# Optimization experiments

Measured on AMD Instinct MI355X. Metric: run time of the kernel, lower is better.

The kernel has to match this reference:

```python
import jax, jax.numpy as jnp
import numpy as np

EMBED_DIM = 128
NUM_SYMBOLS = 200000
PAD_IDX = NUM_SYMBOLS
K_NEIGHBORS = 10
PROCESS_STEPS = 4
D_MODEL = 2 * EMBED_DIM   # 256
D_INNER = 2 * D_MODEL     # 512
LSTM_HID = 2 * D_MODEL    # 512
B, F_SUP, MAX_K = 4096, 5, 64


def setup_inputs() -> dict:
    key = jax.random.key(0)
    ks = jax.random.split(key, 40)
    f = lambda i, shape, s=0.05: jax.random.normal(ks[i], shape, jnp.float32) * s
    inp = {}
    inp['query'] = jax.random.randint(ks[0], (B, 2), 0, NUM_SYMBOLS)
    inp['support'] = jax.random.randint(ks[1], (F_SUP, 2), 0, NUM_SYMBOLS)
    inp['q_l1'] = jax.random.randint(ks[2], (B, MAX_K, 2), 0, NUM_SYMBOLS + 1)
    inp['q_deg_l'] = jax.random.randint(ks[3], (B,), 0, 100)
    inp['q_r1'] = jax.random.randint(ks[4], (B, MAX_K, 2), 0, NUM_SYMBOLS + 1)
    inp['q_deg_r'] = jax.random.randint(ks[5], (B,), 0, 100)
    inp['s_l1'] = jax.random.randint(ks[6], (F_SUP, MAX_K, 2), 0, NUM_SYMBOLS + 1)
    inp['s_deg_l'] = jax.random.randint(ks[7], (F_SUP,), 0, 100)
    inp['s_r1'] = jax.random.randint(ks[8], (F_SUP, MAX_K, 2), 0, NUM_SYMBOLS + 1)
    inp['s_deg_r'] = jax.random.randint(ks[9], (F_SUP,), 0, 100)
    # learned parameters
    inp['symbol_emb'] = f(10, (NUM_SYMBOLS + 1, EMBED_DIM), 0.1).at[PAD_IDX].set(0.0)
    inp['gcn_w_w'] = f(11, (EMBED_DIM, 2 * EMBED_DIM))
    inp['gcn_w_b'] = jnp.zeros((EMBED_DIM,), jnp.float32)
    inp['gcn_b'] = jnp.zeros((EMBED_DIM,), jnp.float32)
    inp['g1_w'] = f(12, (EMBED_DIM // 2, EMBED_DIM))
    inp['g1_b'] = jnp.zeros((EMBED_DIM // 2,), jnp.float32)
    inp['ln1_g'] = jnp.ones((EMBED_DIM // 2,), jnp.float32)
    inp['ln1_b'] = jnp.zeros((EMBED_DIM // 2,), jnp.float32)
    inp['g2_w'] = f(13, (1, EMBED_DIM // 2))
    inp['g2_b'] = jnp.zeros((1,), jnp.float32)
    inp['gate_temp'] = jnp.array(1.0, jnp.float32)
    inp['se_p1_w'] = f(14, (D_INNER, D_MODEL))
    inp['se_p1_b'] = jnp.zeros((D_INNER,), jnp.float32)
    inp['se_p2_w'] = f(15, (D_MODEL, D_INNER))
    inp['se_p2_b'] = jnp.zeros((D_MODEL,), jnp.float32)
    inp['se_ln_g'] = jnp.ones((D_MODEL,), jnp.float32)
    inp['se_ln_b'] = jnp.zeros((D_MODEL,), jnp.float32)
    inp['w_ih'] = f(16, (4 * LSTM_HID, D_MODEL))
    inp['w_hh'] = f(17, (4 * LSTM_HID, LSTM_HID))
    inp['b_ih'] = jnp.zeros((4 * LSTM_HID,), jnp.float32)
    inp['b_hh'] = jnp.zeros((4 * LSTM_HID,), jnp.float32)
    return inp


def _layernorm(x, g, b, eps=1e-5):
    m = jnp.mean(x, axis=-1, keepdims=True)
    v = jnp.var(x, axis=-1, keepdims=True)
    return (x - m) / jnp.sqrt(v + eps) * g + b


def _l2norm(x):
    return x / jnp.maximum(jnp.linalg.norm(x, axis=-1, keepdims=True), 1e-12)


def _neighbor_encoder(conn, deg, self_ids, p):
    emb = p['symbol_emb']
    rel, ent = conn[:, :, 0], conn[:, :, 1]
    rel_emb = emb[rel]            # [n, K, D] gather
    ent_emb = emb[ent]            # [n, K, D]
    self_emb = emb[self_ids]      # [n, D]
    sim = jnp.einsum('nd,nkd->nk', _l2norm(self_emb), _l2norm(ent_emb))
    is_pad = (rel == PAD_IDX).astype(jnp.float32)
    sim = sim - is_pad * 1e9
    k = min(K_NEIGHBORS, conn.shape[1])
    _, k_idx = jax.lax.top_k(sim, k)
    bidx = jnp.arange(conn.shape[0])[:, None]
    k_mask = jnp.zeros(sim.shape, jnp.float32).at[bidx, k_idx].set(1.0)[..., None]
    concat = jnp.concatenate([rel_emb, ent_emb], axis=-1)   # [n, K, 2D]
    proj = jax.nn.leaky_relu(concat @ p['gcn_w_w'].T + p['gcn_w_b'] + p['gcn_b'], 0.01)
    valid = (1.0 - is_pad[..., None]) * k_mask
    denom = jnp.maximum(jnp.sum(valid, axis=1), 1.0)
    agg = jnp.sum((proj * k_mask) * valid, axis=1) / denom   # [n, D]
    h = jax.nn.relu(_layernorm(agg @ p['g1_w'].T + p['g1_b'], p['ln1_g'], p['ln1_b']))
    logit = h @ p['g2_w'].T + p['g2_b']                      # [n, 1]
    temp = jnp.clip(p['gate_temp'], 0.1, 5.0)
    gate = jax.nn.sigmoid(logit / temp) * (deg > 0).astype(jnp.float32)[:, None]
    return jnp.tanh(self_emb + gate * agg)


def _support_encoder(x, p):
    h = jax.nn.relu(x @ p['se_p1_w'].T + p['se_p1_b'])
    h = h @ p['se_p2_w'].T + p['se_p2_b']
    return _layernorm(h + x, p['se_ln_g'], p['se_ln_b'])


def _query_encoder(support, query, p):
    n = query.shape[0]
    h_r0 = jnp.zeros((n, LSTM_HID), jnp.float32)
    c0 = jnp.zeros((n, LSTM_HID), jnp.float32)

    def step(carry, _):
        h_r, c = carry
        gates = query @ p['w_ih'].T + p['b_ih'] + h_r @ p['w_hh'].T + p['b_hh']
        i, f, g, o = jnp.split(gates, 4, axis=-1)
        c = jax.nn.sigmoid(f) * c + jax.nn.sigmoid(i) * jnp.tanh(g)
        h_ = jax.nn.sigmoid(o) * jnp.tanh(c)
        h = query + h_[:, :D_MODEL]
        attn = jax.nn.softmax(h @ support.T, axis=1)
        r = attn @ support
        return (jnp.concatenate([h, r], axis=-1), c), None

    (h_r, _), _ = jax.lax.scan(step, (h_r0, c0), None, length=PROCESS_STEPS)
    return h_r[:, :D_MODEL]


def reference(query, support, q_l1, q_deg_l, q_r1, q_deg_r, s_l1, s_deg_l, s_r1, s_deg_r,
              symbol_emb, gcn_w_w, gcn_w_b, gcn_b, g1_w, g1_b, ln1_g, ln1_b, g2_w, g2_b,
              gate_temp, se_p1_w, se_p1_b, se_p2_w, se_p2_b, se_ln_g, se_ln_b,
              w_ih, w_hh, b_ih, b_hh):
    p = dict(symbol_emb=symbol_emb, gcn_w_w=gcn_w_w, gcn_w_b=gcn_w_b, gcn_b=gcn_b,
             g1_w=g1_w, g1_b=g1_b, ln1_g=ln1_g, ln1_b=ln1_b, g2_w=g2_w, g2_b=g2_b,
             gate_temp=gate_temp, se_p1_w=se_p1_w, se_p1_b=se_p1_b, se_p2_w=se_p2_w,
             se_p2_b=se_p2_b, se_ln_g=se_ln_g, se_ln_b=se_ln_b,
             w_ih=w_ih, w_hh=w_hh, b_ih=b_ih, b_hh=b_hh)
    q_left = _neighbor_encoder(q_l1, q_deg_l, query[:, 0], p)
    q_right = _neighbor_encoder(q_r1, q_deg_r, query[:, 1], p)
    query_vec = jnp.concatenate([q_left, q_right], axis=-1)      # [B, 2D]
    s_left = _neighbor_encoder(s_l1, s_deg_l, support[:, 0], p)
    s_right = _neighbor_encoder(s_r1, s_deg_r, support[:, 1], p)
    support_vec = jnp.concatenate([s_left, s_right], axis=-1)    # [F, 2D]
    support_g = jnp.mean(_support_encoder(support_vec, p), axis=0, keepdims=True)  # [1, 2D]
    query_enc = _support_encoder(query_vec, p)                   # [B, 2D]
    query_g = _query_encoder(support_g, query_enc, p)            # [B, 2D]
    return jnp.sum(query_g * support_g, axis=1)                  # [B]
```

## Files before the change

kernel.cpp:

```cpp
#include <hip/hip_runtime.h>
#include <math.h>

#define BQ 4096
#define F_SUP 5
#define MAXK 64
#define ED 128
#define DM 256
#define DI 512
#define LH 512
#define NG 2048
#define PADX 200000
#define KNB 10
#define MROWS 82048
#define MREAL 82020
#define MQ 4224
#define EMB_ELEMS 25600128
#define NEMB8 3200016

typedef unsigned short u16;
typedef __attribute__((ext_vector_type(8))) short short8;
typedef __attribute__((ext_vector_type(4))) float floatx4;

__device__ __forceinline__ float sigf(float x) { return 1.0f / (1.0f + __expf(-x)); }
__device__ __forceinline__ float tanh_fast(float x) {
  float a = fabsf(x);
  float e = __expf(-2.0f * a);
  float t = (1.0f - e) / (1.0f + e);
  return copysignf(t, x);
}
__device__ __forceinline__ u16 f2bf(float f) {
  unsigned u = __float_as_uint(f);
  unsigned r = (u + 0x7FFFu + ((u >> 16) & 1u)) >> 16;
  return (u16)r;
}
__device__ __forceinline__ float bf2f(u16 u) {
  return __uint_as_float(((unsigned)u) << 16);
}
__device__ __forceinline__ void gl2lds16(const void* g, void* l) {
  __builtin_amdgcn_global_load_lds(
      (const __attribute__((address_space(1))) void*)g,
      (__attribute__((address_space(3))) void*)l, 16, 0, 0);
}

__global__ __launch_bounds__(256) void prep_all(
    const float* __restrict__ emb, u16* __restrict__ embb,
    const float* __restrict__ p1, const float* __restrict__ p2,
    const float* __restrict__ gcnw, const float* __restrict__ wih,
    const float* __restrict__ whh, const float* __restrict__ bih,
    const float* __restrict__ bhh,
    u16* __restrict__ p1b, u16* __restrict__ p2b, u16* __restrict__ gcnb,
    u16* __restrict__ wihb, u16* __restrict__ whhb, float* __restrict__ bihh,
    float* __restrict__ outz)
{
  long gid = (long)blockIdx.x * 256 + threadIdx.x;
  if (gid < (long)NEMB8) {
    long i = gid * 8;
    float4 f0 = *(const float4*)(emb + i);
    float4 f1 = *(const float4*)(emb + i + 4);
    short8 s;
    s[0]=(short)f2bf(f0.x); s[1]=(short)f2bf(f0.y); s[2]=(short)f2bf(f0.z); s[3]=(short)f2bf(f0.w);
    s[4]=(short)f2bf(f1.x); s[5]=(short)f2bf(f1.y); s[6]=(short)f2bf(f1.z); s[7]=(short)f2bf(f1.w);
    *(short8*)(embb + i) = s;
    return;
  }
  int g2 = (int)(gid - NEMB8);
  if (g2 < 131072) { p1b[g2] = f2bf(p1[g2]); }
  else if (g2 < 262144) { int i = g2 - 131072; p2b[i] = f2bf(p2[i]); }
  else if (g2 < 294912) { int i = g2 - 262144; gcnb[i] = f2bf(gcnw[i]); }
  else if (g2 < 819200) {
    int i = g2 - 294912; int p = i >> 8, k = i & 255;
    int g = (p >> 4) & 3, uu = (p >> 7) * 32 + ((p >> 6) & 1) * 16 + (p & 15);
    int n = g * 512 + uu;
    wihb[i] = f2bf(wih[(long)n * DM + k]);
  } else if (g2 < 1343488) {
    int i = g2 - 819200; int p = i >> 8, k = i & 255;
    int g = (p >> 4) & 3, uu = (p >> 7) * 32 + ((p >> 6) & 1) * 16 + (p & 15);
    int n = g * 512 + uu;
    whhb[i] = f2bf(whh[(long)n * LH + k]);
  } else if (g2 < 1345536) {
    int p = g2 - 1343488;
    int g = (p >> 4) & 3, uu = (p >> 7) * 32 + ((p >> 6) & 1) * 16 + (p & 15);
    int n = g * 512 + uu;
    bihh[p] = bih[n] + bhh[n];
  } else if (g2 < 1345536 + BQ) {
    outz[g2 - 1345536] = 0.f;
  }
}

__global__ __launch_bounds__(256) void nbr_simrank_kernel(
    const int* __restrict__ query, const int* __restrict__ support,
    const int* __restrict__ q_l1, const int* __restrict__ q_r1,
    const int* __restrict__ s_l1, const int* __restrict__ s_r1,
    const u16* __restrict__ embb, int* __restrict__ idxA, int* __restrict__ meta)
{
  __shared__ float sE[128];
  __shared__ float simS[64];
  __shared__ int relS[64], entS[64];
  int tid = threadIdx.x;
  int b = blockIdx.x;
  const int* conn; int self_id;
  if (b < BQ)              { int i = b;              conn = q_l1 + (long)i*(MAXK*2); self_id = query[2*i];   }
  else if (b < 2*BQ)       { int i = b - BQ;         conn = q_r1 + (long)i*(MAXK*2); self_id = query[2*i+1]; }
  else if (b < 2*BQ+F_SUP) { int i = b - 2*BQ;       conn = s_l1 + (long)i*(MAXK*2); self_id = support[2*i]; }
  else                     { int i = b - 2*BQ-F_SUP; conn = s_r1 + (long)i*(MAXK*2); self_id = support[2*i+1]; }

  int k = tid >> 2, part = tid & 3;
  int2 rc = *(const int2*)(conn + 2 * k);
  if (tid < 16) {
    short8 s = *(const short8*)(embb + (long)self_id * ED + tid * 8);
    #pragma unroll
    for (int j = 0; j < 8; ++j) sE[tid * 8 + j] = bf2f((u16)s[j]);
  }
  __syncthreads();

  const u16* er = embb + (long)rc.y * ED + part * 8;
  float dot = 0.f, sq = 0.f;
  #pragma unroll
  for (int i = 0; i < 4; ++i) {
    short8 e8 = *(const short8*)(er + i * 32);
    #pragma unroll
    for (int j = 0; j < 8; ++j) {
      float e = bf2f((u16)e8[j]);
      float s = sE[i * 32 + part * 8 + j];
      dot += e * s; sq += e * e;
    }
  }
  dot += __shfl_xor(dot, 1); dot += __shfl_xor(dot, 2);
  sq  += __shfl_xor(sq, 1);  sq  += __shfl_xor(sq, 2);
  if (part == 0) {
    float ne = fmaxf(sqrtf(sq), 1e-12f);
    float sim = dot / ne;
    if (rc.x == PADX) sim -= 1e9f;
    simS[k] = sim; relS[k] = rc.x; entS[k] = rc.y;
  }
  __syncthreads();

  if (tid < 64) {
    float my = simS[tid];
    int rank = 0;
    #pragma unroll
    for (int j = 0; j < 64; ++j) {
      float s = simS[j];
      rank += ((s > my) || (s == my && j < tid)) ? 1 : 0;
    }
    bool val = (rank < KNB) && (relS[tid] != PADX);
    unsigned long long vm = __ballot(val ? 1 : 0);
    int cnt = __popcll(vm);
    long base = (long)b * 10;
    if (val) {
      int pos = __popcll(vm & ((1ull << tid) - 1ull));
      int2 p; p.x = relS[tid]; p.y = entS[tid];
      *(int2*)(idxA + (base + pos) * 2) = p;
    }
    if (tid >= cnt && tid < KNB) {
      int2 pp; pp.x = PADX; pp.y = PADX;
      *(int2*)(idxA + (base + tid) * 2) = pp;
    }
    if (tid == 0) meta[b] = cnt;
  }
  if (b == 0 && tid >= 64 && tid < 64 + 2 * (MROWS - MREAL)) {
    idxA[(long)MREAL * 2 + (tid - 64)] = PADX;
  }
}

__global__ __launch_bounds__(256) void proj_gather_gemm(
    const int* __restrict__ idxA, const u16* __restrict__ embb,
    const u16* __restrict__ W, u16* __restrict__ proj)
{
  __shared__ u16 As[128 * 32];
  __shared__ u16 Bs[128 * 32];
  __shared__ int idxS[256];
  int tid = threadIdx.x;
  int bm = blockIdx.x;
  idxS[tid] = idxA[bm * 256 + tid];
  int lane = tid & 63, wave = tid >> 6;
  int wm = (wave & 1) * 64, wn = (wave >> 1) * 64;
  int col = lane & 15, quad = lane >> 4;

  floatx4 acc[4][4];
  #pragma unroll
  for (int i = 0; i < 4; ++i)
    #pragma unroll
    for (int j = 0; j < 4; ++j) { floatx4 z = {0.f,0.f,0.f,0.f}; acc[i][j] = z; }
  __syncthreads();

  for (int k0 = 0; k0 < 256; k0 += 32) {
    int half = k0 >> 7, koff = k0 & 127;
    #pragma unroll
    for (int t = 0; t < 2; ++t) {
      int c = t * 256 + tid;
      int rb = c >> 2, o = c & 3;
      int og = o ^ (rb & 3);
      gl2lds16(W + (long)rb * 256 + k0 + og * 8, &Bs[(size_t)c * 8]);
      int id = idxS[rb * 2 + half];
      gl2lds16(embb + (long)id * ED + koff + og * 8, &As[(size_t)c * 8]);
    }
    __syncthreads();
    short8 af[4], bfr[4];
    #pragma unroll
    for (int i = 0; i < 4; ++i) {
      int ra = wm + i * 16 + col;
      af[i] = *(const short8*)&As[(size_t)(ra * 4 + (quad ^ (ra & 3))) * 8];
      int rb = wn + i * 16 + col;
      bfr[i] = *(const short8*)&Bs[(size_t)(rb * 4 + (quad ^ (rb & 3))) * 8];
    }
    #pragma unroll
    for (int i = 0; i < 4; ++i)
      #pragma unroll
      for (int j = 0; j < 4; ++j)
        acc[i][j] = __builtin_amdgcn_mfma_f32_16x16x32_bf16(af[i], bfr[j], acc[i][j], 0, 0, 0);
    __syncthreads();
  }
  int gm0 = bm * 128 + wm + quad * 4;
  int gn0 = wn + col;
  #pragma unroll
  for (int i = 0; i < 4; ++i)
    #pragma unroll
    for (int j = 0; j < 4; ++j)
      #pragma unroll
      for (int rr = 0; rr < 4; ++rr)
        proj[(long)(gm0 + i * 16 + rr) * 128 + gn0 + j * 16] = f2bf(acc[i][j][rr]);
}

__global__ __launch_bounds__(128) void nbr_post_kernel(
    const int* __restrict__ query, const int* __restrict__ support,
    const int* __restrict__ q_deg_l, const int* __restrict__ q_deg_r,
    const int* __restrict__ s_deg_l, const int* __restrict__ s_deg_r,
    const float* __restrict__ emb,
    const u16* __restrict__ proj, const int* __restrict__ meta,
    const float* __restrict__ gcn_w_b, const float* __restrict__ gcn_b,
    const float* __restrict__ g1_w, const float* __restrict__ g1_b,
    const float* __restrict__ ln1_g, const float* __restrict__ ln1_b,
    const float* __restrict__ g2_w, const float* __restrict__ g2_b,
    const float* __restrict__ gate_temp,
    float* __restrict__ qv, u16* __restrict__ qv_bf)
{
  __shared__ __align__(16) float aggS[128];
  __shared__ float sEs[128];
  __shared__ float gateS;
  int tid = threadIdx.x, b = blockIdx.x;
  int deg, self_id, row, colb;
  if (b < BQ)              { int i = b;              deg = q_deg_l[i]; self_id = query[2*i];     row = i;        colb = 0;  }
  else if (b < 2*BQ)       { int i = b - BQ;         deg = q_deg_r[i]; self_id = query[2*i+1];   row = i;        colb = ED; }
  else if (b < 2*BQ+F_SUP) { int i = b - 2*BQ;       deg = s_deg_l[i]; self_id = support[2*i];   row = BQ + i;   colb = 0;  }
  else                     { int i = b - 2*BQ-F_SUP; deg = s_deg_r[i]; self_id = support[2*i+1]; row = BQ + i;   colb = ED; }
  float* outp = qv + (long)row * DM + colb;
  u16*  outpb = qv_bf + (long)row * DM + colb;

  int cnt = meta[b];
  float denom = fmaxf((float)cnt, 1.0f);
  float bsum = gcn_w_b[tid] + gcn_b[tid];
  float agg = 0.f;
  long pbase = (long)b * 10;
  for (int kk = 0; kk < cnt; ++kk) {
    float z = bf2f(proj[(pbase + kk) * 128 + tid]) + bsum;
    z = (z >= 0.f) ? z : 0.01f * z;
    agg += z;
  }
  agg /= denom;
  aggS[tid] = agg;
  sEs[tid] = emb[(long)self_id * ED + tid];
  __syncthreads();

  if (tid < 64) {
    int e = tid;
    const float4* g1r = (const float4*)(g1_w + e * ED);
    float y = g1_b[e];
    #pragma unroll 8
    for (int j = 0; j < 32; ++j) {
      float4 w = g1r[j];
      float4 a = *(const float4*)&aggS[j * 4];
      y += w.x*a.x + w.y*a.y + w.z*a.z + w.w*a.w;
    }
    float s = y;
    #pragma unroll
    for (int off = 1; off < 64; off <<= 1) s += __shfl_xor(s, off);
    float mean = s * (1.0f / 64.0f);
    float dv = y - mean;
    float s2 = dv * dv;
    #pragma unroll
    for (int off = 1; off < 64; off <<= 1) s2 += __shfl_xor(s2, off);
    float var = s2 * (1.0f / 64.0f);
    float hv = dv / sqrtf(var + 1e-5f) * ln1_g[e] + ln1_b[e];
    hv = fmaxf(hv, 0.f);
    float lp = hv * g2_w[e];
    #pragma unroll
    for (int off = 1; off < 64; off <<= 1) lp += __shfl_xor(lp, off);
    if (e == 0) {
      float logit = lp + g2_b[0];
      float temp = fminf(fmaxf(gate_temp[0], 0.1f), 5.0f);
      float gate = 1.0f / (1.0f + expf(-logit / temp));
      if (deg <= 0) gate = 0.f;
      gateS = gate;
    }
  }
  __syncthreads();
  float o = tanhf(sEs[tid] + gateS * aggS[tid]);
  outp[tid] = o;
  outpb[tid] = f2bf(o);
}

__global__ __launch_bounds__(256) void mfma_gemm(
    const u16* __restrict__ A, int lda,
    const u16* __restrict__ W, int ldw,
    int N, int K,
    float* __restrict__ Cout, u16* __restrict__ Cbf,
    const float* __restrict__ bias0,
    const u16* __restrict__ gqin,
    u16* __restrict__ gqout,
    int relu, int lstm_mode,
    float* __restrict__ cstate, const float* __restrict__ qe,
    u16* __restrict__ hbf,
    const float* __restrict__ whh_f, float* __restrict__ sgo, float* __restrict__ sco)
{
  __shared__ u16 As[128 * 32];
  __shared__ u16 Bs[128 * 32];
  int tid = threadIdx.x;

  if (lstm_mode == 2 && whh_f && blockIdx.x >= gridDim.x - 512) {
    int sc = blockIdx.x - (gridDim.x - 512);
    float* sgS = (float*)As;
    float v = 0.f;
    #pragma unroll
    for (int r = 0; r < F_SUP; ++r) v += qe[(long)(BQ + r) * DM + tid];
    v *= (1.0f / (float)F_SUP);
    sgS[tid] = v;
    if (sc == 0) sgo[tid] = v;
    __syncthreads();
    int wv = tid >> 6, lane = tid & 63;
    int n = sc * 4 + wv;
    float4 w = *(const float4*)(whh_f + (long)n * LH + DM + lane * 4);
    float4 s = *(const float4*)&sgS[lane * 4];
    float d = w.x*s.x + w.y*s.y + w.z*s.z + w.w*s.w;
    #pragma unroll
    for (int off = 1; off < 64; off <<= 1) d += __shfl_xor(d, off);
    if (lane == 0) {
      int g = n >> 9, uu = n & 511;
      int p = (uu >> 5) * 128 + ((uu >> 4) & 1) * 64 + g * 16 + (uu & 15);
      sco[p] = d;
    }
    return;
  }

  int nb = N >> 7;
  int bn = blockIdx.x % nb, bm = blockIdx.x / nb;
  int lane = tid & 63, wave = tid >> 6;
  int wm = (wave & 1) * 64, wn = (wave >> 1) * 64;
  int col = lane & 15, quad = lane >> 4;

  u16 gqa[64]; float cpv[16]; float qev[16]; float scv[4];
  int u = 0; long fb = 0;
  if (lstm_mode) {
    u = bn * 32 + (wave >> 1) * 16 + col;
    fb = ((long)(bm * (NG >> 7) + bn) * 4 + wave) * 64 + lane;
    #pragma unroll
    for (int j = 0; j < 4; ++j)
      scv[j] = bias0[bn * 128 + (wave >> 1) * 64 + j * 16 + col];
    if (lstm_mode == 1) {
      const short8* gp = (const short8*)(gqin + fb * 64);
      #pragma unroll
      for (int t = 0; t < 8; ++t) *(short8*)&gqa[t * 8] = gp[t];
      const float4* cp = (const float4*)(cstate + fb * 16);
      #pragma unroll
      for (int t = 0; t < 4; ++t) *(float4*)&cpv[t * 4] = cp[t];
    }
    if (u < DM) {
      #pragma unroll
      for (int i = 0; i < 4; ++i)
        #pragma unroll
        for (int r = 0; r < 4; ++r) {
          int m = bm * 128 + (wave & 1) * 64 + i * 16 + quad * 4 + r;
          qev[i * 4 + r] = qe[(long)m * DM + u];
        }
    }
  }

  floatx4 acc[4][4];
  #pragma unroll
  for (int i = 0; i < 4; ++i)
    #pragma unroll
    for (int j = 0; j < 4; ++j) { floatx4 z = {0.f,0.f,0.f,0.f}; acc[i][j] = z; }

  for (int k0 = 0; k0 < K; k0 += 32) {
    #pragma unroll
    for (int t = 0; t < 2; ++t) {
      int c = t * 256 + tid;
      int r = c >> 2, o = c & 3;
      int og = o ^ (r & 3);
      gl2lds16(A + (long)(bm * 128 + r) * lda + k0 + og * 8, &As[(size_t)c * 8]);
      gl2lds16(W + (long)(bn * 128 + r) * ldw + k0 + og * 8, &Bs[(size_t)c * 8]);
    }
    __syncthreads();
    short8 af[4], bfr[4];
    #pragma unroll
    for (int i = 0; i < 4; ++i) {
      int ra = wm + i * 16 + col;
      af[i] = *(const short8*)&As[(size_t)(ra * 4 + (quad ^ (ra & 3))) * 8];
      int rb = wn + i * 16 + col;
      bfr[i] = *(const short8*)&Bs[(size_t)(rb * 4 + (quad ^ (rb & 3))) * 8];
    }
    #pragma unroll
    for (int i = 0; i < 4; ++i)
      #pragma unroll
      for (int j = 0; j < 4; ++j)
        acc[i][j] = __builtin_amdgcn_mfma_f32_16x16x32_bf16(af[i], bfr[j], acc[i][j], 0, 0, 0);
    __syncthreads();
  }

  if (lstm_mode) {
    float cnew[16];
    #pragma unroll
    for (int i = 0; i < 4; ++i) {
      #pragma unroll
      for (int r = 0; r < 4; ++r) {
        float gI = acc[i][0][r] + scv[0];
        float gF = acc[i][1][r] + scv[1];
        float gG = acc[i][2][r] + scv[2];
        float gO = acc[i][3][r] + scv[3];
        if (lstm_mode == 1) {
          gI += bf2f(gqa[(i * 4 + 0) * 4 + r]);
          gF += bf2f(gqa[(i * 4 + 1) * 4 + r]);
          gG += bf2f(gqa[(i * 4 + 2) * 4 + r]);
          gO += bf2f(gqa[(i * 4 + 3) * 4 + r]);
        }
        float cp = (lstm_mode == 2) ? 0.f : cpv[i * 4 + r];
        float cn = sigf(gF) * cp + sigf(gI) * tanh_fast(gG);
        cnew[i * 4 + r] = cn;
        if (u < DM) {
          int m = bm * 128 + (wave & 1) * 64 + i * 16 + quad * 4 + r;
          hbf[(long)m * DM + u] = f2bf(qev[i * 4 + r] + sigf(gO) * tanh_fast(cn));
        }
      }
    }
    {
      float4* cp = (float4*)(cstate + fb * 16);
      #pragma unroll
      for (int t = 0; t < 4; ++t) cp[t] = *(float4*)&cnew[t * 4];
    }
    if (lstm_mode == 2) {
      u16 ga[64];
      #pragma unroll
      for (int i = 0; i < 4; ++i)
        #pragma unroll
        for (int j = 0; j < 4; ++j)
          #pragma unroll
          for (int r = 0; r < 4; ++r)
            ga[(i * 4 + j) * 4 + r] = f2bf(acc[i][j][r] + scv[j]);
      short8* gp = (short8*)(gqout + fb * 64);
      #pragma unroll
      for (int t = 0; t < 8; ++t) gp[t] = *(short8*)&ga[t * 8];
    }
  } else {
    int gm0 = bm * 128 + wm + quad * 4;
    int gn0 = bn * 128 + wn + col;
    #pragma unroll
    for (int i = 0; i < 4; ++i) {
      #pragma unroll
      for (int j = 0; j < 4; ++j) {
        int n = gn0 + j * 16;
        #pragma unroll
        for (int r = 0; r < 4; ++r) {
          int m = gm0 + i * 16 + r;
          float v = acc[i][j][r];
          if (bias0) v += bias0[n];
          if (relu) v = fmaxf(v, 0.f);
          if (Cout) Cout[(long)m * N + n] = v;
          if (Cbf)  Cbf[(long)m * N + n] = f2bf(v);
        }
      }
    }
  }
}

__global__ __launch_bounds__(256) void lstm4_dot_kernel(
    const u16* __restrict__ A,
    const u16* __restrict__ W,
    const float* __restrict__ bias0,
    const u16* __restrict__ gqin, const float* __restrict__ cstate,
    const float* __restrict__ qe, const float* __restrict__ sgv,
    float* __restrict__ dotv)
{
  __shared__ u16 As[64 * 32];
  __shared__ u16 Bs[128 * 32];
  int tid = threadIdx.x;
  int bn = blockIdx.x & 7, bm = blockIdx.x >> 3;
  int lane = tid & 63, wave = tid >> 6;
  int col = lane & 15, quad = (lane >> 4) & 3;
  int w1 = wave & 1, w2 = wave >> 1;

  int u = bn * 32 + w2 * 16 + col;
  long fb = (((long)(bm >> 1) * 16 + bn) * 4 + ((bm & 1) | (w2 << 1))) * 64 + lane;
  float scv[4], qev[8], cpv[8]; u16 gqa[32];
  #pragma unroll
  for (int j = 0; j < 4; ++j)
    scv[j] = bias0[bn * 128 + w2 * 64 + j * 16 + col];
  {
    const short8* gp = (const short8*)(gqin + fb * 64);
    const float4* cp = (const float4*)(cstate + fb * 16);
    #pragma unroll
    for (int i = 0; i < 2; ++i) {
      int io = w1 * 2 + i;
      *(short8*)&gqa[i * 16]     = gp[io * 2];
      *(short8*)&gqa[i * 16 + 8] = gp[io * 2 + 1];
      *(float4*)&cpv[i * 4]      = cp[io];
    }
    #pragma unroll
    for (int i = 0; i < 2; ++i)
      #pragma unroll
      for (int r = 0; r < 4; ++r) {
        int m = bm * 64 + w1 * 32 + i * 16 + quad * 4 + r;
        qev[i * 4 + r] = qe[(long)m * DM + u];
      }
  }
  float sgu = sgv[u];

  floatx4 acc[2][4];
  #pragma unroll
  for (int i = 0; i < 2; ++i)
    #pragma unroll
    for (int j = 0; j < 4; ++j) { floatx4 z = {0.f,0.f,0.f,0.f}; acc[i][j] = z; }

  for (int k0 = 0; k0 < 256; k0 += 32) {
    {
      int r = tid >> 2, o = tid & 3;
      int og = o ^ (r & 3);
      gl2lds16(A + (long)(bm * 64 + r) * DM + k0 + og * 8, &As[(size_t)tid * 8]);
    }
    #pragma unroll
    for (int t = 0; t < 2; ++t) {
      int c = t * 256 + tid;
      int r = c >> 2, o = c & 3;
      int og = o ^ (r & 3);
      gl2lds16(W + (long)(bn * 128 + r) * DM + k0 + og * 8, &Bs[(size_t)c * 8]);
    }
    __syncthreads();
    short8 af[2], bfr[4];
    #pragma unroll
    for (int i = 0; i < 2; ++i) {
      int ra = w1 * 32 + i * 16 + col;
      af[i] = *(const short8*)&As[(size_t)(ra * 4 + (quad ^ (ra & 3))) * 8];
    }
    #pragma unroll
    for (int j = 0; j < 4; ++j) {
      int rb = w2 * 64 + j * 16 + col;
      bfr[j] = *(const short8*)&Bs[(size_t)(rb * 4 + (quad ^ (rb & 3))) * 8];
    }
    #pragma unroll
    for (int i = 0; i < 2; ++i)
      #pragma unroll
      for (int j = 0; j < 4; ++j)
        acc[i][j] = __builtin_amdgcn_mfma_f32_16x16x32_bf16(af[i], bfr[j], acc[i][j], 0, 0, 0);
    __syncthreads();
  }

  #pragma unroll
  for (int i = 0; i < 2; ++i) {
    #pragma unroll
    for (int r = 0; r < 4; ++r) {
      float gI = acc[i][0][r] + scv[0] + bf2f(gqa[i * 16 + 0 * 4 + r]);
      float gF = acc[i][1][r] + scv[1] + bf2f(gqa[i * 16 + 1 * 4 + r]);
      float gG = acc[i][2][r] + scv[2] + bf2f(gqa[i * 16 + 2 * 4 + r]);
      float gO = acc[i][3][r] + scv[3] + bf2f(gqa[i * 16 + 3 * 4 + r]);
      float cn = sigf(gF) * cpv[i * 4 + r] + sigf(gI) * tanh_fast(gG);
      float hv = qev[i * 4 + r] + sigf(gO) * tanh_fast(cn);
      float p = hv * sgu;
      p += __shfl_xor(p, 1); p += __shfl_xor(p, 2);
      p += __shfl_xor(p, 4); p += __shfl_xor(p, 8);
      if (col == 0) {
        int m = bm * 64 + w1 * 32 + i * 16 + quad * 4 + r;
        atomicAdd(&dotv[m], p);
      }
    }
  }
}

__global__ __launch_bounds__(256) void ln_residual_kernel(
    const float* __restrict__ h2buf, const float* __restrict__ xbuf,
    const float* __restrict__ lng, const float* __restrict__ lnb,
    float* __restrict__ out, u16* __restrict__ outb)
{
  __shared__ float red[4];
  int r = blockIdx.x, tid = threadIdx.x;
  float v = h2buf[(long)r * DM + tid] + xbuf[(long)r * DM + tid];
  float s = v;
  #pragma unroll
  for (int off = 1; off < 64; off <<= 1) s += __shfl_xor(s, off);
  if ((tid & 63) == 0) red[tid >> 6] = s;
  __syncthreads();
  float mean = (red[0] + red[1] + red[2] + red[3]) * (1.0f / 256.0f);
  __syncthreads();
  float dv = v - mean;
  float s2 = dv * dv;
  #pragma unroll
  for (int off = 1; off < 64; off <<= 1) s2 += __shfl_xor(s2, off);
  if ((tid & 63) == 0) red[tid >> 6] = s2;
  __syncthreads();
  float var = (red[0] + red[1] + red[2] + red[3]) * (1.0f / 256.0f);
  float o = dv / sqrtf(var + 1e-5f) * lng[tid] + lnb[tid];
  out[(long)r * DM + tid] = o;
  outb[(long)r * DM + tid] = f2bf(o);
}

extern "C" void kernel_launch(void* const* d_in, const int* in_sizes, int n_in,
                              void* d_out, int out_size, void* d_ws, size_t ws_size,
                              hipStream_t stream)
{
  const int*   query    = (const int*)  d_in[0];
  const int*   support  = (const int*)  d_in[1];
  const int*   q_l1     = (const int*)  d_in[2];
  const int*   q_deg_l  = (const int*)  d_in[3];
  const int*   q_r1     = (const int*)  d_in[4];
  const int*   q_deg_r  = (const int*)  d_in[5];
  const int*   s_l1     = (const int*)  d_in[6];
  const int*   s_deg_l  = (const int*)  d_in[7];
  const int*   s_r1     = (const int*)  d_in[8];
  const int*   s_deg_r  = (const int*)  d_in[9];
  const float* symbol_emb = (const float*)d_in[10];
  const float* gcn_w_w  = (const float*)d_in[11];
  const float* gcn_w_b  = (const float*)d_in[12];
  const float* gcn_b    = (const float*)d_in[13];
  const float* g1_w     = (const float*)d_in[14];
  const float* g1_b     = (const float*)d_in[15];
  const float* ln1_g    = (const float*)d_in[16];
  const float* ln1_b    = (const float*)d_in[17];
  const float* g2_w     = (const float*)d_in[18];
  const float* g2_b     = (const float*)d_in[19];
  const float* gate_temp= (const float*)d_in[20];
  const float* se_p1_w  = (const float*)d_in[21];
  const float* se_p1_b  = (const float*)d_in[22];
  const float* se_p2_w  = (const float*)d_in[23];
  const float* se_p2_b  = (const float*)d_in[24];
  const float* se_ln_g  = (const float*)d_in[25];
  const float* se_ln_b  = (const float*)d_in[26];
  const float* w_ih     = (const float*)d_in[27];
  const float* w_hh     = (const float*)d_in[28];
  const float* b_ih     = (const float*)d_in[29];
  const float* b_hh     = (const float*)d_in[30];

  float* ws = (float*)d_ws;
  size_t off = 0;
  float* projF   = ws + off; off += (size_t)MROWS * 128 / 2;
  float* idxF    = ws + off; off += (size_t)MROWS * 2;
  float* qv      = ws + off; off += (size_t)MQ * DM;
  float* qe      = ws + off; off += (size_t)MQ * DM;
  float* qv_bfF  = ws + off; off += (size_t)MQ * DM / 2;
  float* qe_bfF  = ws + off; off += (size_t)MQ * DM / 2;
  float* h1bF    = ws + off; off += (size_t)MQ * DI / 2;
  float* H2      = ws + off; off += (size_t)MQ * DM;
  float* gqbF    = ws + off; off += (size_t)BQ * NG / 2;
  float* cstate  = ws + off; off += (size_t)BQ * LH;
  float* hbf0F   = ws + off; off += (size_t)BQ * DM / 2;
  float* hbf1F   = ws + off; off += (size_t)BQ * DM / 2;
  float* p1bF    = ws + off; off += 131072 / 2;
  float* p2bF    = ws + off; off += 131072 / 2;
  float* gcnbF   = ws + off; off += 32768 / 2;
  float* wihbF   = ws + off; off += 524288 / 2;
  float* whhbF   = ws + off; off += 524288 / 2;
  float* bihh    = ws + off; off += 2048;
  float* sg      = ws + off; off += 256;
  float* s_corr  = ws + off; off += 2048;
  float* metaF   = ws + off; off += 8448;
  float* embbF   = ws + off; off += (size_t)EMB_ELEMS / 2;

  u16* proj   = (u16*)projF;
  int* idxA   = (int*)idxF;
  u16* qv_bf  = (u16*)qv_bfF;
  u16* qe_bf  = (u16*)qe_bfF;
  u16* H1_bf  = (u16*)h1bF;
  u16* gq_fr  = (u16*)gqbF;
  u16* hbf0   = (u16*)hbf0F;
  u16* hbf1   = (u16*)hbf1F;
  u16* p1b    = (u16*)p1bF;
  u16* p2b    = (u16*)p2bF;
  u16* gcnb   = (u16*)gcnbF;
  u16* wihb   = (u16*)wihbF;
  u16* whhb   = (u16*)whhbF;
  int* meta   = (int*)metaF;
  u16* embb   = (u16*)embbF;

  {
    long total = (long)NEMB8 + 1345536 + BQ;
    int blocks = (int)((total + 255) / 256);
    prep_all<<<blocks, 256, 0, stream>>>(symbol_emb, embb,
        se_p1_w, se_p2_w, gcn_w_w, w_ih, w_hh, b_ih, b_hh,
        p1b, p2b, gcnb, wihb, whhb, bihh, (float*)d_out);
  }

  nbr_simrank_kernel<<<2 * BQ + 2 * F_SUP, 256, 0, stream>>>(
      query, support, q_l1, q_r1, s_l1, s_r1, embb, idxA, meta);

  proj_gather_gemm<<<MROWS / 128, 256, 0, stream>>>(idxA, embb, gcnb, proj);

  nbr_post_kernel<<<2 * BQ + 2 * F_SUP, 128, 0, stream>>>(
      query, support, q_deg_l, q_deg_r, s_deg_l, s_deg_r, symbol_emb,
      proj, meta, gcn_w_b, gcn_b, g1_w, g1_b, ln1_g, ln1_b, g2_w, g2_b, gate_temp,
      qv, qv_bf);

  mfma_gemm<<<(MQ / 128) * (DI / 128), 256, 0, stream>>>(qv_bf, 256, p1b, 256, DI, 256,
      nullptr, H1_bf, se_p1_b, nullptr, nullptr, 1, 0, nullptr, nullptr, nullptr,
      nullptr, nullptr, nullptr);
  mfma_gemm<<<(MQ / 128) * (DM / 128), 256, 0, stream>>>(H1_bf, 512, p2b, 512, DM, 512,
      H2, nullptr, se_p2_b, nullptr, nullptr, 0, 0, nullptr, nullptr, nullptr,
      nullptr, nullptr, nullptr);
  ln_residual_kernel<<<BQ + F_SUP, 256, 0, stream>>>(H2, qv, se_ln_g, se_ln_b, qe, qe_bf);

  mfma_gemm<<<(BQ / 128) * (NG / 128) + 512, 256, 0, stream>>>(qe_bf, 256, wihb, 256, NG, 256,
      nullptr, nullptr, bihh, nullptr, gq_fr, 0, 2, cstate, qe, hbf0,
      w_hh, sg, s_corr);

  mfma_gemm<<<(BQ / 128) * (NG / 128), 256, 0, stream>>>(hbf0, 256, whhb, 256, NG, 256,
      nullptr, nullptr, s_corr, gq_fr, nullptr, 0, 1, cstate, qe, hbf1,
      nullptr, nullptr, nullptr);
  mfma_gemm<<<(BQ / 128) * (NG / 128), 256, 0, stream>>>(hbf1, 256, whhb, 256, NG, 256,
      nullptr, nullptr, s_corr, gq_fr, nullptr, 0, 1, cstate, qe, hbf0,
      nullptr, nullptr, nullptr);

  lstm4_dot_kernel<<<(BQ / 64) * 8, 256, 0, stream>>>(hbf0, whhb, s_corr,
      gq_fr, cstate, qe, sg, (float*)d_out);
}
```

Before: 415.5 us.

## Fuse neighbor projection GEMM with aggregation and gating epilogue

Merges the gather-projection GEMM and the per-entity neighbor post-processing into one kernel. Each block now handles 12 entities (120 rows, padded to 128) and keeps the projected tile in swizzled shared memory instead of writing it to global memory. The aggregation, gate MLP and tanh output then run in the same block. This removes the global proj buffer round trip and one kernel launch. In exchange it wastes a few rows per tile, raises LDS usage (which may cut occupancy), and runs the gate computation with only 4 waves per block.

```diff
diff --git a/kernel.cpp b/kernel.cpp
--- a/kernel.cpp
+++ b/kernel.cpp
@@ -11,8 +11,10 @@
 #define NG 2048
 #define PADX 200000
 #define KNB 10
-#define MROWS 82048
-#define MREAL 82020
+#define NBTOT 8202
+#define BPB 12
+#define NPBLK 684
+#define MPAD 82080
 #define MQ 4224
 #define EMB_ELEMS 25600128
 #define NEMB8 3200016
@@ -158,21 +160,34 @@
     }
     if (tid == 0) meta[b] = cnt;
   }
-  if (b == 0 && tid >= 64 && tid < 64 + 2 * (MROWS - MREAL)) {
-    idxA[(long)MREAL * 2 + (tid - 64)] = PADX;
-  }
-}
-
-__global__ __launch_bounds__(256) void proj_gather_gemm(
+  if (b == 0 && tid >= 64 && tid < 64 + 2 * (MPAD - NBTOT * 10)) {
+    idxA[(long)(NBTOT * 10) * 2 + (tid - 64)] = PADX;
+  }
+}
+
+__global__ __launch_bounds__(256) void proj_agg_kernel(
     const int* __restrict__ idxA, const u16* __restrict__ embb,
-    const u16* __restrict__ W, u16* __restrict__ proj)
+    const u16* __restrict__ W, const int* __restrict__ meta,
+    const int* __restrict__ query, const int* __restrict__ support,
+    const int* __restrict__ q_deg_l, const int* __restrict__ q_deg_r,
+    const int* __restrict__ s_deg_l, const int* __restrict__ s_deg_r,
+    const float* __restrict__ emb,
+    const float* __restrict__ gcn_w_b, const float* __restrict__ gcn_b,
+    const float* __restrict__ g1_w, const float* __restrict__ g1_b,
+    const float* __restrict__ ln1_g, const float* __restrict__ ln1_b,
+    const float* __restrict__ g2_w, const float* __restrict__ g2_b,
+    const float* __restrict__ gate_temp,
+    float* __restrict__ qv, u16* __restrict__ qv_bf)
 {
   __shared__ u16 As[128 * 32];
   __shared__ u16 Bs[128 * 32];
+  __shared__ u16 Ps[128 * 128];
+  __shared__ float aggS[BPB * 128];
+  __shared__ float gateS[BPB];
   __shared__ int idxS[256];
   int tid = threadIdx.x;
   int bm = blockIdx.x;
-  idxS[tid] = idxA[bm * 256 + tid];
+  idxS[tid] = (tid < 240) ? idxA[bm * 240 + tid] : PADX;
   int lane = tid & 63, wave = tid >> 6;
   int wm = (wave & 1) * 64, wn = (wave >> 1) * 64;
   int col = lane & 15, quad = lane >> 4;
@@ -211,93 +226,103 @@
         acc[i][j] = __builtin_amdgcn_mfma_f32_16x16x32_bf16(af[i], bfr[j], acc[i][j], 0, 0, 0);
     __syncthreads();
   }
-  int gm0 = bm * 128 + wm + quad * 4;
-  int gn0 = wn + col;
-  #pragma unroll
-  for (int i = 0; i < 4; ++i)
-    #pragma unroll
-    for (int j = 0; j < 4; ++j)
-      #pragma unroll
-      for (int rr = 0; rr < 4; ++rr)
-        proj[(long)(gm0 + i * 16 + rr) * 128 + gn0 + j * 16] = f2bf(acc[i][j][rr]);
-}
-
-__global__ __launch_bounds__(128) void nbr_post_kernel(
-    const int* __restrict__ query, const int* __restrict__ support,
-    const int* __restrict__ q_deg_l, const int* __restrict__ q_deg_r,
-    const int* __restrict__ s_deg_l, const int* __restrict__ s_deg_r,
-    const float* __restrict__ emb,
-    const u16* __restrict__ proj, const int* __restrict__ meta,
-    const float* __restrict__ gcn_w_b, const float* __restrict__ gcn_b,
-    const float* __restrict__ g1_w, const float* __restrict__ g1_b,
-    const float* __restrict__ ln1_g, const float* __restrict__ ln1_b,
-    const float* __restrict__ g2_w, const float* __restrict__ g2_b,
-    const float* __restrict__ gate_temp,
-    float* __restrict__ qv, u16* __restrict__ qv_bf)
-{
-  __shared__ __align__(16) float aggS[128];
-  __shared__ float sEs[128];
-  __shared__ float gateS;
-  int tid = threadIdx.x, b = blockIdx.x;
-  int deg, self_id, row, colb;
-  if (b < BQ)              { int i = b;              deg = q_deg_l[i]; self_id = query[2*i];     row = i;        colb = 0;  }
-  else if (b < 2*BQ)       { int i = b - BQ;         deg = q_deg_r[i]; self_id = query[2*i+1];   row = i;        colb = ED; }
-  else if (b < 2*BQ+F_SUP) { int i = b - 2*BQ;       deg = s_deg_l[i]; self_id = support[2*i];   row = BQ + i;   colb = 0;  }
-  else                     { int i = b - 2*BQ-F_SUP; deg = s_deg_r[i]; self_id = support[2*i+1]; row = BQ + i;   colb = ED; }
-  float* outp = qv + (long)row * DM + colb;
-  u16*  outpb = qv_bf + (long)row * DM + colb;
-
-  int cnt = meta[b];
-  float denom = fmaxf((float)cnt, 1.0f);
-  float bsum = gcn_w_b[tid] + gcn_b[tid];
-  float agg = 0.f;
-  long pbase = (long)b * 10;
-  for (int kk = 0; kk < cnt; ++kk) {
-    float z = bf2f(proj[(pbase + kk) * 128 + tid]) + bsum;
-    z = (z >= 0.f) ? z : 0.01f * z;
-    agg += z;
-  }
-  agg /= denom;
-  aggS[tid] = agg;
-  sEs[tid] = emb[(long)self_id * ED + tid];
-  __syncthreads();
-
-  if (tid < 64) {
-    int e = tid;
-    const float4* g1r = (const float4*)(g1_w + e * ED);
-    float y = g1_b[e];
-    #pragma unroll 8
-    for (int j = 0; j < 32; ++j) {
-      float4 w = g1r[j];
-      float4 a = *(const float4*)&aggS[j * 4];
-      y += w.x*a.x + w.y*a.y + w.z*a.z + w.w*a.w;
-    }
-    float s = y;
-    #pragma unroll
-    for (int off = 1; off < 64; off <<= 1) s += __shfl_xor(s, off);
-    float mean = s * (1.0f / 64.0f);
-    float dv = y - mean;
-    float s2 = dv * dv;
-    #pragma unroll
-    for (int off = 1; off < 64; off <<= 1) s2 += __shfl_xor(s2, off);
-    float var = s2 * (1.0f / 64.0f);
-    float hv = dv / sqrtf(var + 1e-5f) * ln1_g[e] + ln1_b[e];
-    hv = fmaxf(hv, 0.f);
-    float lp = hv * g2_w[e];
-    #pragma unroll
-    for (int off = 1; off < 64; off <<= 1) lp += __shfl_xor(lp, off);
-    if (e == 0) {
-      float logit = lp + g2_b[0];
-      float temp = fminf(fmaxf(gate_temp[0], 0.1f), 5.0f);
-      float gate = 1.0f / (1.0f + expf(-logit / temp));
-      if (deg <= 0) gate = 0.f;
-      gateS = gate;
-    }
-  }
-  __syncthreads();
-  float o = tanhf(sEs[tid] + gateS * aggS[tid]);
-  outp[tid] = o;
-  outpb[tid] = f2bf(o);
+
+  {
+    int gm0 = wm + quad * 4, gn0 = wn + col;
+    #pragma unroll
+    for (int i = 0; i < 4; ++i)
+      #pragma unroll
+      for (int j = 0; j < 4; ++j)
+        #pragma unroll
+        for (int rr = 0; rr < 4; ++rr) {
+          int row = gm0 + i * 16 + rr, cn = gn0 + j * 16;
+          Ps[(size_t)((row * 128 + cn) ^ ((row & 7) << 3))] = f2bf(acc[i][j][rr]);
+        }
+  }
+  __syncthreads();
+
+  {
+    int half = tid >> 7, c = tid & 127;
+    float bsum = gcn_w_b[c] + gcn_b[c];
+    #pragma unroll
+    for (int bb0 = 0; bb0 < 6; ++bb0) {
+      int bb = bb0 * 2 + half;
+      int b = bm * BPB + bb;
+      int cnt = (b < NBTOT) ? meta[b] : 0;
+      float agg = 0.f;
+      for (int kk = 0; kk < cnt; ++kk) {
+        int row = bb * 10 + kk;
+        float z = bf2f(Ps[(size_t)((row * 128 + c) ^ ((row & 7) << 3))]) + bsum;
+        z = (z >= 0.f) ? z : 0.01f * z;
+        agg += z;
+      }
+      agg /= fmaxf((float)cnt, 1.0f);
+      aggS[bb * 128 + c] = agg;
+    }
+  }
+  __syncthreads();
+
+  for (int t = 0; t < 3; ++t) {
+    int bb = wave + t * 4;
+    int b = bm * BPB + bb;
+    if (b < NBTOT) {
+      int deg;
+      if (b < BQ)              deg = q_deg_l[b];
+      else if (b < 2*BQ)       deg = q_deg_r[b - BQ];
+      else if (b < 2*BQ+F_SUP) deg = s_deg_l[b - 2*BQ];
+      else                     deg = s_deg_r[b - 2*BQ - F_SUP];
+      int e = lane;
+      const float4* g1r = (const float4*)(g1_w + e * ED);
+      const float4* ag  = (const float4*)&aggS[bb * 128];
+      float y = g1_b[e];
+      #pragma unroll 8
+      for (int j = 0; j < 32; ++j) {
+        float4 w4 = g1r[j];
+        float4 a4 = ag[j];
+        y += w4.x*a4.x + w4.y*a4.y + w4.z*a4.z + w4.w*a4.w;
+      }
+      float s = y;
+      #pragma unroll
+      for (int off = 1; off < 64; off <<= 1) s += __shfl_xor(s, off);
+      float mean = s * (1.0f / 64.0f);
+      float dv = y - mean;
+      float s2 = dv * dv;
+      #pragma unroll
+      for (int off = 1; off < 64; off <<= 1) s2 += __shfl_xor(s2, off);
+      float var = s2 * (1.0f / 64.0f);
+      float hv = dv / sqrtf(var + 1e-5f) * ln1_g[e] + ln1_b[e];
+      hv = fmaxf(hv, 0.f);
+      float lp = hv * g2_w[e];
+      #pragma unroll
+      for (int off = 1; off < 64; off <<= 1) lp += __shfl_xor(lp, off);
+      if (e == 0) {
+        float logit = lp + g2_b[0];
+        float temp = fminf(fmaxf(gate_temp[0], 0.1f), 5.0f);
+        float gate = 1.0f / (1.0f + expf(-logit / temp));
+        if (deg <= 0) gate = 0.f;
+        gateS[bb] = gate;
+      }
+    }
+  }
+  __syncthreads();
+
+  {
+    int half = tid >> 7, c = tid & 127;
+    #pragma unroll
+    for (int bb0 = 0; bb0 < 6; ++bb0) {
+      int bb = bb0 * 2 + half;
+      int b = bm * BPB + bb;
+      if (b >= NBTOT) continue;
+      int self_id, row, colb;
+      if (b < BQ)              { int i = b;              self_id = query[2*i];     row = i;        colb = 0;  }
+      else if (b < 2*BQ)       { int i = b - BQ;         self_id = query[2*i+1];   row = i;        colb = ED; }
+      else if (b < 2*BQ+F_SUP) { int i = b - 2*BQ;       self_id = support[2*i];   row = BQ + i;   colb = 0;  }
+      else                     { int i = b - 2*BQ-F_SUP; self_id = support[2*i+1]; row = BQ + i;   colb = ED; }
+      float o = tanhf(emb[(long)self_id * ED + c] + gateS[bb] * aggS[bb * 128 + c]);
+      qv[(long)row * DM + colb + c] = o;
+      qv_bf[(long)row * DM + colb + c] = f2bf(o);
+    }
+  }
 }
 
 __global__ __launch_bounds__(256) void mfma_gemm(
@@ -639,8 +664,7 @@
 
   float* ws = (float*)d_ws;
   size_t off = 0;
-  float* projF   = ws + off; off += (size_t)MROWS * 128 / 2;
-  float* idxF    = ws + off; off += (size_t)MROWS * 2;
+  float* idxF    = ws + off; off += (size_t)MPAD * 2 + 64;
   float* qv      = ws + off; off += (size_t)MQ * DM;
   float* qe      = ws + off; off += (size_t)MQ * DM;
   float* qv_bfF  = ws + off; off += (size_t)MQ * DM / 2;
@@ -662,7 +686,6 @@
   float* metaF   = ws + off; off += 8448;
   float* embbF   = ws + off; off += (size_t)EMB_ELEMS / 2;
 
-  u16* proj   = (u16*)projF;
   int* idxA   = (int*)idxF;
   u16* qv_bf  = (u16*)qv_bfF;
   u16* qe_bf  = (u16*)qe_bfF;
@@ -686,14 +709,12 @@
         p1b, p2b, gcnb, wihb, whhb, bihh, (float*)d_out);
   }
 
-  nbr_simrank_kernel<<<2 * BQ + 2 * F_SUP, 256, 0, stream>>>(
+  nbr_simrank_kernel<<<NBTOT, 256, 0, stream>>>(
       query, support, q_l1, q_r1, s_l1, s_r1, embb, idxA, meta);
 
-  proj_gather_gemm<<<MROWS / 128, 256, 0, stream>>>(idxA, embb, gcnb, proj);
-
-  nbr_post_kernel<<<2 * BQ + 2 * F_SUP, 128, 0, stream>>>(
+  proj_agg_kernel<<<NPBLK, 256, 0, stream>>>(idxA, embb, gcnb, meta,
       query, support, q_deg_l, q_deg_r, s_deg_l, s_deg_r, symbol_emb,
-      proj, meta, gcn_w_b, gcn_b, g1_w, g1_b, ln1_g, ln1_b, g2_w, g2_b, gate_temp,
+      gcn_w_b, gcn_b, g1_w, g1_b, ln1_g, ln1_b, g2_w, g2_b, gate_temp,
       qv, qv_bf);
 
   mfma_gemm<<<(MQ / 128) * (DI / 128), 256, 0, stream>>>(qv_bf, 256, p1b, 256, DI, 256,
```

Result: slower. 427.5 us (+2.9%).
